# Optimization experiments

Measured on AMD Instinct MI355X. Metric: run time of the kernel, lower is better.

The kernel has to match this reference:

```python
import jax, jax.numpy as jnp
import numpy as np
from jax import lax

DN = ('NCHW', 'OIHW', 'NCHW')
EPS = 1e-9
MASK_THR = 1e-3


def box_filter(x, size):
    # Separable box (ones) filter with SAME padding; x: [1,1,H,W]
    pad = size // 2
    kv = jnp.ones((1, 1, size, 1), x.dtype)
    kh = jnp.ones((1, 1, 1, size), x.dtype)
    y = lax.conv_general_dilated(x, kv, (1, 1), [(pad, pad), (0, 0)], dimension_numbers=DN)
    return lax.conv_general_dilated(y, kh, (1, 1), [(0, 0), (pad, pad)], dimension_numbers=DN)


def setup_inputs() -> dict:
    key = jax.random.key(0)
    k1, k2, k3, k4 = jax.random.split(key, 4)
    H = W = 2048
    I = jax.random.uniform(k1, (1, 1, H, W), jnp.float32)            # image in [0,1]
    u = jax.random.uniform(k2, (1, 4, H, W), jnp.float32)            # class memberships
    b = 1.0 + 0.1 * jax.random.normal(k3, (1, 1, H, W), jnp.float32)  # bias field ~1
    e = jax.random.normal(k4, (1, 1, H, W), jnp.float32) * 0.1       # residual
    return {"I": I, "u": u, "b": b, "e": e, "p": 2, "size": 21}


def reference(I, u, b, e, p, size):
    C = u.shape[1]
    e_d = lax.stop_gradient(e)
    b_d = lax.stop_gradient(b)
    up = u ** p                      # [1,C,H,W]
    b2 = b_d * b_d
    mask = (I > MASK_THR).astype(I.dtype)
    norm = box_filter(mask, size)    # partialFilter: local valid-pixel count

    def filt(x):                     # convParFilt: mask-normalized local mean
        return box_filter(x, size) / (norm + EPS)

    b_K = filt(b)
    b2_K = filt(b2)

    # classCenter (vectorized over classes 1..C-1)
    A = (I - e_d) * b_K                                   # [1,1,H,W]
    num = jnp.sum(A * up[:, 1:], axis=(0, 2, 3))          # [C-1]
    den = jnp.sum(b2_K * up[:, 1:], axis=(0, 2, 3))       # [C-1]
    c0 = jnp.sum(I * up[:, :1]) / (jnp.sum(up[:, :1]) + EPS)
    v = jnp.concatenate([c0[None], num / (den + EPS)])    # [C]

    # bias-field update: convolution is linear, so sum over classes first
    vb = v[None, :, None, None]
    bd = filt((I - e_d) * jnp.sum(vb * up, axis=1, keepdims=True))
    db = filt(jnp.sum(vb * vb * up, axis=1, keepdims=True))
    bd = bd * mask + (1.0 - mask)
    db = db * mask + (1.0 - mask)
    b_new = bd / (db + EPS)
    diff = b - b_new
    return jnp.mean(diff * diff)
```

## Files before the change

### kernel.cpp

```cpp
#include <hip/hip_runtime.h>

constexpr int Hh = 2048;
constexpr int Ww = 2048;
constexpr int NN = Hh * Ww;
constexpr int W4 = Ww / 4;
constexpr int NN4 = NN / 4;
constexpr int RAD = 10;
constexpr float EPSf = 1e-9f;
constexpr float MASK_THRf = 0.001f;
constexpr int CH = 8;
constexpr int BH = 16;
constexpr int NB = Hh / BH;
constexpr int TOTW = NB * Ww;
constexpr int NSLOT = 32;

__device__ inline float rcpf(float x) { return __builtin_amdgcn_rcpf(x); }

__device__ inline float waveReduce(float v) {
    #pragma unroll
    for (int o = 32; o > 0; o >>= 1) v += __shfl_down(v, o, 64);
    return v;
}

__device__ inline float4 f4zero() { float4 z; z.x = z.y = z.z = z.w = 0.f; return z; }
__device__ inline float4 f4add(float4 a, float4 b) {
    float4 r; r.x = a.x + b.x; r.y = a.y + b.y; r.z = a.z + b.z; r.w = a.w + b.w; return r;
}
__device__ inline float4 f4sub(float4 a, float4 b) {
    float4 r; r.x = a.x - b.x; r.y = a.y - b.y; r.z = a.z - b.z; r.w = a.w - b.w; return r;
}
__device__ inline void add4(float4& a, const float4 b) { a.x += b.x; a.y += b.y; a.z += b.z; a.w += b.w; }

__device__ inline void scan4(float v0, float v1, float v2, float v3, int lane,
                             float& carry, float P[4]) {
    float s0 = v0, s1 = s0 + v1, s2 = s1 + v2, s3 = s2 + v3;
    float T = s3;
    #pragma unroll
    for (int o = 1; o < 64; o <<= 1) {
        float t = __shfl_up(T, o, 64);
        if (lane >= o) T += t;
    }
    float base = T - s3 + carry;
    P[0] = base + s0; P[1] = base + s1; P[2] = base + s2; P[3] = base + s3;
    carry += __shfl(T, 63, 64);
}

__device__ inline float4 boxExtract(const float Pp[4], const float Pc[4], const float Pn[4], int lane) {
    int l2 = (lane + 2) & 63, l3 = (lane + 3) & 63;
    int m3 = (lane - 3) & 63, m2 = (lane - 2) & 63;
    bool c2 = (lane + 2) < 64, c3 = (lane + 3) < 64;
    bool g3 = lane >= 3, g2 = lane >= 2;
    float hc0 = __shfl(Pc[2], l2, 64), hn0 = __shfl(Pn[2], l2, 64);
    float hc1 = __shfl(Pc[3], l2, 64), hn1 = __shfl(Pn[3], l2, 64);
    float hc2 = __shfl(Pc[0], l3, 64), hn2 = __shfl(Pn[0], l3, 64);
    float hc3 = __shfl(Pc[1], l3, 64), hn3 = __shfl(Pn[1], l3, 64);
    float lc0 = __shfl(Pc[1], m3, 64), lp0 = __shfl(Pp[1], m3, 64);
    float lc1 = __shfl(Pc[2], m3, 64), lp1 = __shfl(Pp[2], m3, 64);
    float lc2 = __shfl(Pc[3], m3, 64), lp2 = __shfl(Pp[3], m3, 64);
    float lc3 = __shfl(Pc[0], m2, 64), lp3 = __shfl(Pp[0], m2, 64);
    float4 r;
    r.x = (c2 ? hc0 : hn0) - (g3 ? lc0 : lp0);
    r.y = (c2 ? hc1 : hn1) - (g3 ? lc1 : lp1);
    r.z = (c3 ? hc2 : hn2) - (g3 ? lc2 : lp2);
    r.w = (c3 ? hc3 : hn3) - (g2 ? lc3 : lp3);
    return r;
}

__global__ __launch_bounds__(256) void k1p(
        const float* __restrict__ I, const float* __restrict__ B,
        float* __restrict__ vpm, float* __restrict__ vpb, float* __restrict__ vpb2,
        float* __restrict__ tm, float* __restrict__ tb, float* __restrict__ tb2) {
    int x4 = blockIdx.x * 256 + threadIdx.x;
    int y0 = blockIdx.y * BH;
    const float4* I4 = (const float4*)I;
    const float4* B4 = (const float4*)B;
    float4 am = f4zero(), ab = f4zero(), ab2 = f4zero();
    #pragma unroll
    for (int r = 0; r < BH; ++r) {
        int idx = (y0 + r) * W4 + x4;
        float4 iv = I4[idx], bv = B4[idx];
        am.x += (iv.x > MASK_THRf) ? 1.f : 0.f;
        am.y += (iv.y > MASK_THRf) ? 1.f : 0.f;
        am.z += (iv.z > MASK_THRf) ? 1.f : 0.f;
        am.w += (iv.w > MASK_THRf) ? 1.f : 0.f;
        ab.x += bv.x; ab.y += bv.y; ab.z += bv.z; ab.w += bv.w;
        ab2.x += bv.x * bv.x; ab2.y += bv.y * bv.y;
        ab2.z += bv.z * bv.z; ab2.w += bv.w * bv.w;
        ((float4*)vpm)[idx] = am;
        ((float4*)vpb)[idx] = ab;
        ((float4*)vpb2)[idx] = ab2;
    }
    int t = blockIdx.y * W4 + x4;
    ((float4*)tm)[t] = am; ((float4*)tb)[t] = ab; ((float4*)tb2)[t] = ab2;
}

__global__ __launch_bounds__(256) void koff(
        const float* __restrict__ t0, const float* __restrict__ t1, const float* __restrict__ t2,
        float* __restrict__ o0, float* __restrict__ o1, float* __restrict__ o2) {
    int col = blockIdx.x * 256 + threadIdx.x;
    const float4* t; float4* o;
    if (blockIdx.y == 0)      { t = (const float4*)t0; o = (float4*)o0; }
    else if (blockIdx.y == 1) { t = (const float4*)t1; o = (float4*)o1; }
    else                      { t = (const float4*)t2; o = (float4*)o2; }
    float4 acc = f4zero();
    #pragma unroll 8
    for (int b = 0; b < NB; ++b) {
        o[b * W4 + col] = acc;
        float4 v = t[b * W4 + col];
        add4(acc, v);
    }
}

#define VBOX3(cc, vA, vB, vC, PA, PB, PC, OA, OB, OC) do { \
    int xo_ = (cc) * 64 + lane; \
    float4 uA_ = PA[upBase + xo_], uB_ = PB[upBase + xo_], uC_ = PC[upBase + xo_]; \
    float4 oA_ = OA[obUp + xo_], oB_ = OB[obUp + xo_], oC_ = OC[obUp + xo_]; \
    float4 dA_ = f4zero(), dB_ = f4zero(), dC_ = f4zero(); \
    float4 eA_ = f4zero(), eB_ = f4zero(), eC_ = f4zero(); \
    if (hasDn) { dA_ = PA[dnBase + xo_]; dB_ = PB[dnBase + xo_]; dC_ = PC[dnBase + xo_]; \
                 eA_ = OA[obDn + xo_]; eB_ = OB[obDn + xo_]; eC_ = OC[obDn + xo_]; } \
    vA = f4sub(f4add(uA_, oA_), f4add(dA_, eA_)); \
    vB = f4sub(f4add(uB_, oB_), f4add(dB_, eB_)); \
    vC = f4sub(f4add(uC_, oC_), f4add(dC_, eC_)); } while (0)

__device__ inline void k2_pix(float bm, float bb, float bb2, float Iv, float ev,
                              float u0, float u1, float u2, float u3, float* a) {
    float rn = rcpf(bm + EPSf);
    float bK = bb * rn;
    float b2K = bb2 * rn;
    float p0 = u0 * u0, p1 = u1 * u1, p2 = u2 * u2, p3 = u3 * u3;
    a[0] += Iv * p0;
    a[1] += p0;
    float A = (Iv - ev) * bK;
    a[2] += A * p1; a[3] += A * p2; a[4] += A * p3;
    a[5] += b2K * p1; a[6] += b2K * p2; a[7] += b2K * p3;
}

__global__ __launch_bounds__(256) void k2h(
        const float* __restrict__ vpm, const float* __restrict__ vpb, const float* __restrict__ vpb2,
        const float* __restrict__ om, const float* __restrict__ ob, const float* __restrict__ ob2,
        const float* __restrict__ I, const float* __restrict__ E, const float* __restrict__ U,
        float* __restrict__ accA) {
    int row = (blockIdx.x * 256 + threadIdx.x) >> 6;
    int lane = threadIdx.x & 63;
    int yup = row + RAD; if (yup > Hh - 1) yup = Hh - 1;
    int ydn = row - RAD - 1;
    bool hasDn = ydn >= 0;
    int upBase = yup * W4;
    int dnBase = hasDn ? ydn * W4 : 0;
    int obUp = (yup / BH) * W4;
    int obDn = hasDn ? (ydn / BH) * W4 : 0;
    int rowBase = row * W4;

    const float4* Pm = (const float4*)vpm;
    const float4* Pb = (const float4*)vpb;
    const float4* Pq = (const float4*)vpb2;
    const float4* Om = (const float4*)om;
    const float4* Ob = (const float4*)ob;
    const float4* Oq = (const float4*)ob2;
    const float4* I4 = (const float4*)I;
    const float4* E4 = (const float4*)E;
    const float4* U0 = (const float4*)U;
    const float4* U1 = U0 + NN4;
    const float4* U2 = U1 + NN4;
    const float4* U3 = U2 + NN4;

    float cm = 0.f, cb = 0.f, cq = 0.f;
    float Pm_p[4] = {0, 0, 0, 0}, Pb_p[4] = {0, 0, 0, 0}, Pq_p[4] = {0, 0, 0, 0};
    float Pm_c[4], Pb_c[4], Pq_c[4], Pm_n[4], Pb_n[4], Pq_n[4];
    float a[8] = {0, 0, 0, 0, 0, 0, 0, 0};

    {
        float4 vm, vb, vq;
        VBOX3(0, vm, vb, vq, Pm, Pb, Pq, Om, Ob, Oq);
        scan4(vm.x, vm.y, vm.z, vm.w, lane, cm, Pm_c);
        scan4(vb.x, vb.y, vb.z, vb.w, lane, cb, Pb_c);
        scan4(vq.x, vq.y, vq.z, vq.w, lane, cq, Pq_c);
    }
    #pragma unroll 1
    for (int c = 0; c < CH; ++c) {
        int xo = rowBase + c * 64 + lane;
        float4 Iv = I4[xo], Ev = E4[xo];
        float4 u0 = U0[xo], u1 = U1[xo], u2 = U2[xo], u3 = U3[xo];
        if (c + 1 < CH) {
            float4 vm, vb, vq;
            VBOX3(c + 1, vm, vb, vq, Pm, Pb, Pq, Om, Ob, Oq);
            scan4(vm.x, vm.y, vm.z, vm.w, lane, cm, Pm_n);
            scan4(vb.x, vb.y, vb.z, vb.w, lane, cb, Pb_n);
            scan4(vq.x, vq.y, vq.z, vq.w, lane, cq, Pq_n);
        } else {
            #pragma unroll
            for (int e = 0; e < 4; ++e) { Pm_n[e] = cm; Pb_n[e] = cb; Pq_n[e] = cq; }
        }
        float4 bm = boxExtract(Pm_p, Pm_c, Pm_n, lane);
        float4 bb = boxExtract(Pb_p, Pb_c, Pb_n, lane);
        float4 bq = boxExtract(Pq_p, Pq_c, Pq_n, lane);
        k2_pix(bm.x, bb.x, bq.x, Iv.x, Ev.x, u0.x, u1.x, u2.x, u3.x, a);
        k2_pix(bm.y, bb.y, bq.y, Iv.y, Ev.y, u0.y, u1.y, u2.y, u3.y, a);
        k2_pix(bm.z, bb.z, bq.z, Iv.z, Ev.z, u0.z, u1.z, u2.z, u3.z, a);
        k2_pix(bm.w, bb.w, bq.w, Iv.w, Ev.w, u0.w, u1.w, u2.w, u3.w, a);
        #pragma unroll
        for (int e = 0; e < 4; ++e) {
            Pm_p[e] = Pm_c[e]; Pb_p[e] = Pb_c[e]; Pq_p[e] = Pq_c[e];
            Pm_c[e] = Pm_n[e]; Pb_c[e] = Pb_n[e]; Pq_c[e] = Pq_n[e];
        }
    }

    __shared__ float sred[4][8];
    int wave = threadIdx.x >> 6;
    #pragma unroll
    for (int k = 0; k < 8; ++k) a[k] = waveReduce(a[k]);
    if (lane == 0) {
        #pragma unroll
        for (int k = 0; k < 8; ++k) sred[wave][k] = a[k];
    }
    __syncthreads();
    if (threadIdx.x < 8) {
        float s = sred[0][threadIdx.x] + sred[1][threadIdx.x] +
                  sred[2][threadIdx.x] + sred[3][threadIdx.x];
        atomicAdd(&accA[threadIdx.x * NSLOT + (blockIdx.x & (NSLOT - 1))], s);
    }
}

__global__ void k3_v(const float* __restrict__ accA, float* __restrict__ vV) {
    int lane = threadIdx.x;
    float s[8];
    #pragma unroll
    for (int k = 0; k < 8; ++k) {
        float v = (lane < NSLOT) ? accA[k * NSLOT + lane] : 0.f;
        s[k] = waveReduce(v);
    }
    if (lane == 0) {
        vV[0] = s[0] / (s[1] + EPSf);
        vV[1] = s[2] / (s[5] + EPSf);
        vV[2] = s[3] / (s[6] + EPSf);
        vV[3] = s[4] / (s[7] + EPSf);
    }
}

__global__ __launch_bounds__(256) void k4p(
        const float* __restrict__ I, const float* __restrict__ E, const float* __restrict__ U,
        const float* __restrict__ vV,
        float* __restrict__ vpP, float* __restrict__ vpQ,
        float* __restrict__ tP, float* __restrict__ tQ) {
    int x4 = blockIdx.x * 256 + threadIdx.x;
    int y0 = blockIdx.y * BH;
    float v0 = vV[0], v1 = vV[1], v2 = vV[2], v3 = vV[3];
    float w0 = v0 * v0, w1 = v1 * v1, w2 = v2 * v2, w3 = v3 * v3;
    const float4* I4 = (const float4*)I;
    const float4* E4 = (const float4*)E;
    const float4* U0 = (const float4*)U;
    const float4* U1 = U0 + NN4;
    const float4* U2 = U1 + NN4;
    const float4* U3 = U2 + NN4;
    float4 aP = f4zero(), aQ = f4zero();
    #pragma unroll
    for (int r = 0; r < BH; ++r) {
        int idx = (y0 + r) * W4 + x4;
        float4 Iv = I4[idx], Ev = E4[idx];
        float4 a0 = U0[idx], a1 = U1[idx], a2 = U2[idx], a3 = U3[idx];
        float p0, p1, p2, p3;
        p0 = a0.x * a0.x; p1 = a1.x * a1.x; p2 = a2.x * a2.x; p3 = a3.x * a3.x;
        aP.x += (Iv.x - Ev.x) * (v0 * p0 + v1 * p1 + v2 * p2 + v3 * p3);
        aQ.x += w0 * p0 + w1 * p1 + w2 * p2 + w3 * p3;
        p0 = a0.y * a0.y; p1 = a1.y * a1.y; p2 = a2.y * a2.y; p3 = a3.y * a3.y;
        aP.y += (Iv.y - Ev.y) * (v0 * p0 + v1 * p1 + v2 * p2 + v3 * p3);
        aQ.y += w0 * p0 + w1 * p1 + w2 * p2 + w3 * p3;
        p0 = a0.z * a0.z; p1 = a1.z * a1.z; p2 = a2.z * a2.z; p3 = a3.z * a3.z;
        aP.z += (Iv.z - Ev.z) * (v0 * p0 + v1 * p1 + v2 * p2 + v3 * p3);
        aQ.z += w0 * p0 + w1 * p1 + w2 * p2 + w3 * p3;
        p0 = a0.w * a0.w; p1 = a1.w * a1.w; p2 = a2.w * a2.w; p3 = a3.w * a3.w;
        aP.w += (Iv.w - Ev.w) * (v0 * p0 + v1 * p1 + v2 * p2 + v3 * p3);
        aQ.w += w0 * p0 + w1 * p1 + w2 * p2 + w3 * p3;
        ((float4*)vpP)[idx] = aP;
        ((float4*)vpQ)[idx] = aQ;
    }
    int t = blockIdx.y * W4 + x4;
    ((float4*)tP)[t] = aP; ((float4*)tQ)[t] = aQ;
}

__global__ __launch_bounds__(256) void k5h(
        const float* __restrict__ vpP, const float* __restrict__ vpQ, const float* __restrict__ vpm,
        const float* __restrict__ oP, const float* __restrict__ oQ, const float* __restrict__ om,
        const float* __restrict__ I, const float* __restrict__ B,
        float* __restrict__ accL) {
    int row = (blockIdx.x * 256 + threadIdx.x) >> 6;
    int lane = threadIdx.x & 63;
    int yup = row + RAD; if (yup > Hh - 1) yup = Hh - 1;
    int ydn = row - RAD - 1;
    bool hasDn = ydn >= 0;
    int upBase = yup * W4;
    int dnBase = hasDn ? ydn * W4 : 0;
    int obUp = (yup / BH) * W4;
    int obDn = hasDn ? (ydn / BH) * W4 : 0;
    int rowBase = row * W4;

    const float4* Pp4 = (const float4*)vpP;
    const float4* Pq4 = (const float4*)vpQ;
    const float4* Pm4 = (const float4*)vpm;
    const float4* Op4 = (const float4*)oP;
    const float4* Oq4 = (const float4*)oQ;
    const float4* Om4 = (const float4*)om;
    const float4* I4 = (const float4*)I;
    const float4* B4 = (const float4*)B;

    float cP = 0.f, cQ = 0.f, cm = 0.f;
    float PP_p[4] = {0, 0, 0, 0}, PQ_p[4] = {0, 0, 0, 0}, PM_p[4] = {0, 0, 0, 0};
    float PP_c[4], PQ_c[4], PM_c[4], PP_n[4], PQ_n[4], PM_n[4];
    float a = 0.f;

    {
        float4 vP, vQ, vm;
        VBOX3(0, vP, vQ, vm, Pp4, Pq4, Pm4, Op4, Oq4, Om4);
        scan4(vP.x, vP.y, vP.z, vP.w, lane, cP, PP_c);
        scan4(vQ.x, vQ.y, vQ.z, vQ.w, lane, cQ, PQ_c);
        scan4(vm.x, vm.y, vm.z, vm.w, lane, cm, PM_c);
    }
    #pragma unroll 1
    for (int c = 0; c < CH; ++c) {
        int xo = rowBase + c * 64 + lane;
        float4 Iv = I4[xo], Bv = B4[xo];
        if (c + 1 < CH) {
            float4 vP, vQ, vm;
            VBOX3(c + 1, vP, vQ, vm, Pp4, Pq4, Pm4, Op4, Oq4, Om4);
            scan4(vP.x, vP.y, vP.z, vP.w, lane, cP, PP_n);
            scan4(vQ.x, vQ.y, vQ.z, vQ.w, lane, cQ, PQ_n);
            scan4(vm.x, vm.y, vm.z, vm.w, lane, cm, PM_n);
        } else {
            #pragma unroll
            for (int e = 0; e < 4; ++e) { PP_n[e] = cP; PQ_n[e] = cQ; PM_n[e] = cm; }
        }
        float4 bP = boxExtract(PP_p, PP_c, PP_n, lane);
        float4 bQ = boxExtract(PQ_p, PQ_c, PQ_n, lane);
        float4 bM = boxExtract(PM_p, PM_c, PM_n, lane);
        {
            float rn = rcpf(bM.x + EPSf);
            float bd = bP.x * rn, db = bQ.x * rn;
            float m = (Iv.x > MASK_THRf) ? 1.f : 0.f;
            bd = bd * m + (1.f - m); db = db * m + (1.f - m);
            float d = Bv.x - bd * rcpf(db + EPSf); a += d * d;
        }
        {
            float rn = rcpf(bM.y + EPSf);
            float bd = bP.y * rn, db = bQ.y * rn;
            float m = (Iv.y > MASK_THRf) ? 1.f : 0.f;
            bd = bd * m + (1.f - m); db = db * m + (1.f - m);
            float d = Bv.y - bd * rcpf(db + EPSf); a += d * d;
        }
        {
            float rn = rcpf(bM.z + EPSf);
            float bd = bP.z * rn, db = bQ.z * rn;
            float m = (Iv.z > MASK_THRf) ? 1.f : 0.f;
            bd = bd * m + (1.f - m); db = db * m + (1.f - m);
            float d = Bv.z - bd * rcpf(db + EPSf); a += d * d;
        }
        {
            float rn = rcpf(bM.w + EPSf);
            float bd = bP.w * rn, db = bQ.w * rn;
            float m = (Iv.w > MASK_THRf) ? 1.f : 0.f;
            bd = bd * m + (1.f - m); db = db * m + (1.f - m);
            float d = Bv.w - bd * rcpf(db + EPSf); a += d * d;
        }
        #pragma unroll
        for (int e = 0; e < 4; ++e) {
            PP_p[e] = PP_c[e]; PQ_p[e] = PQ_c[e]; PM_p[e] = PM_c[e];
            PP_c[e] = PP_n[e]; PQ_c[e] = PQ_n[e]; PM_c[e] = PM_n[e];
        }
    }

    a = waveReduce(a);
    __shared__ float sred[4];
    int wave = threadIdx.x >> 6;
    if (lane == 0) sred[wave] = a;
    __syncthreads();
    if (threadIdx.x == 0) {
        atomicAdd(&accL[blockIdx.x & (NSLOT - 1)], sred[0] + sred[1] + sred[2] + sred[3]);
    }
}

__global__ void k6_out(const float* __restrict__ accL, float* __restrict__ out) {
    int lane = threadIdx.x;
    float v = (lane < NSLOT) ? accL[lane] : 0.f;
    v = waveReduce(v);
    if (lane == 0) out[0] = v / (float)NN;
}

extern "C" void kernel_launch(void* const* d_in, const int* in_sizes, int n_in,
                              void* d_out, int out_size, void* d_ws, size_t ws_size,
                              hipStream_t stream) {
    const float* I = (const float*)d_in[0];
    const float* U = (const float*)d_in[1];
    const float* B = (const float*)d_in[2];
    const float* E = (const float*)d_in[3];

    float* vpm  = (float*)d_ws;
    float* vpb  = vpm + NN;
    float* vpb2 = vpb + NN;
    float* tm   = vpb2 + NN;
    float* tb   = tm + TOTW;
    float* tb2  = tb + TOTW;
    float* om   = tb2 + TOTW;
    float* ob   = om + TOTW;
    float* ob2  = ob + TOTW;
    float* accA = ob2 + TOTW;
    float* accL = accA + 8 * NSLOT;
    float* vV   = accL + NSLOT;

    hipMemsetAsync(accA, 0, (8 * NSLOT + NSLOT) * sizeof(float), stream);

    dim3 blk(256);
    dim3 gband(2, NB);
    int hblocks = Hh / 4;

    k1p<<<gband, blk, 0, stream>>>(I, B, vpm, vpb, vpb2, tm, tb, tb2);
    koff<<<dim3(2, 3), blk, 0, stream>>>(tm, tb, tb2, om, ob, ob2);
    k2h<<<hblocks, blk, 0, stream>>>(vpm, vpb, vpb2, om, ob, ob2, I, E, U, accA);
    k3_v<<<1, 64, 0, stream>>>(accA, vV);
    k4p<<<gband, blk, 0, stream>>>(I, E, U, vV, vpb, vpb2, tm, tb);
    koff<<<dim3(2, 2), blk, 0, stream>>>(tm, tb, tb2, ob, ob2, om);
    k5h<<<hblocks, blk, 0, stream>>>(vpb, vpb2, vpm, ob, ob2, om, I, B, accL);
    k6_out<<<1, 64, 0, stream>>>(accL, (float*)d_out);
}
```

Baseline: 238.9 us.

## Split each row's horizontal box pass across two waves and halve band height

The horizontal box/reduction kernels now give each row to two waves instead of one. Each wave handles half of the column chunks, and the second wave rebuilds the preceding chunk's prefix so its window stays correct. Band height drops from 16 to 8, and the offset prefix kernel now works in place, which removes the separate offset buffers. The goal is more wave-level parallelism and latency hiding in the main passes. The cost is some redundant neighbour-chunk loads and scans, plus a longer serial loop in the offset kernel.

```diff
diff --git a/kernel.cpp b/kernel.cpp
--- a/kernel.cpp
+++ b/kernel.cpp
@@ -9,7 +9,8 @@
 constexpr float EPSf = 1e-9f;
 constexpr float MASK_THRf = 0.001f;
 constexpr int CH = 8;
-constexpr int BH = 16;
+constexpr int SEGC = CH / 2;
+constexpr int BH = 8;
 constexpr int NB = Hh / BH;
 constexpr int TOTW = NB * Ww;
 constexpr int NSLOT = 32;
@@ -95,18 +96,17 @@
 }
 
 __global__ __launch_bounds__(256) void koff(
-        const float* __restrict__ t0, const float* __restrict__ t1, const float* __restrict__ t2,
-        float* __restrict__ o0, float* __restrict__ o1, float* __restrict__ o2) {
+        float* __restrict__ t0, float* __restrict__ t1, float* __restrict__ t2) {
     int col = blockIdx.x * 256 + threadIdx.x;
-    const float4* t; float4* o;
-    if (blockIdx.y == 0)      { t = (const float4*)t0; o = (float4*)o0; }
-    else if (blockIdx.y == 1) { t = (const float4*)t1; o = (float4*)o1; }
-    else                      { t = (const float4*)t2; o = (float4*)o2; }
+    float4* t;
+    if (blockIdx.y == 0)      t = (float4*)t0;
+    else if (blockIdx.y == 1) t = (float4*)t1;
+    else                      t = (float4*)t2;
     float4 acc = f4zero();
     #pragma unroll 8
     for (int b = 0; b < NB; ++b) {
-        o[b * W4 + col] = acc;
         float4 v = t[b * W4 + col];
+        t[b * W4 + col] = acc;
         add4(acc, v);
     }
 }
@@ -141,8 +141,11 @@
         const float* __restrict__ om, const float* __restrict__ ob, const float* __restrict__ ob2,
         const float* __restrict__ I, const float* __restrict__ E, const float* __restrict__ U,
         float* __restrict__ accA) {
-    int row = (blockIdx.x * 256 + threadIdx.x) >> 6;
+    int wid = (blockIdx.x * 256 + threadIdx.x) >> 6;
     int lane = threadIdx.x & 63;
+    int row = wid >> 1;
+    int seg = wid & 1;
+    int c0 = seg * SEGC;
     int yup = row + RAD; if (yup > Hh - 1) yup = Hh - 1;
     int ydn = row - RAD - 1;
     bool hasDn = ydn >= 0;
@@ -170,15 +173,23 @@
     float Pm_c[4], Pb_c[4], Pq_c[4], Pm_n[4], Pb_n[4], Pq_n[4];
     float a[8] = {0, 0, 0, 0, 0, 0, 0, 0};
 
+    if (seg > 0) {
+        float4 vm, vb, vq;
+        VBOX3(c0 - 1, vm, vb, vq, Pm, Pb, Pq, Om, Ob, Oq);
+        scan4(vm.x, vm.y, vm.z, vm.w, lane, cm, Pm_p);
+        scan4(vb.x, vb.y, vb.z, vb.w, lane, cb, Pb_p);
+        scan4(vq.x, vq.y, vq.z, vq.w, lane, cq, Pq_p);
+    }
     {
         float4 vm, vb, vq;
-        VBOX3(0, vm, vb, vq, Pm, Pb, Pq, Om, Ob, Oq);
+        VBOX3(c0, vm, vb, vq, Pm, Pb, Pq, Om, Ob, Oq);
         scan4(vm.x, vm.y, vm.z, vm.w, lane, cm, Pm_c);
         scan4(vb.x, vb.y, vb.z, vb.w, lane, cb, Pb_c);
         scan4(vq.x, vq.y, vq.z, vq.w, lane, cq, Pq_c);
     }
-    #pragma unroll 1
-    for (int c = 0; c < CH; ++c) {
+    #pragma unroll
+    for (int cc = 0; cc < SEGC; ++cc) {
+        int c = c0 + cc;
         int xo = rowBase + c * 64 + lane;
         float4 Iv = I4[xo], Ev = E4[xo];
         float4 u0 = U0[xo], u1 = U1[xo], u2 = U2[xo], u3 = U3[xo];
@@ -284,8 +295,11 @@
         const float* __restrict__ oP, const float* __restrict__ oQ, const float* __restrict__ om,
         const float* __restrict__ I, const float* __restrict__ B,
         float* __restrict__ accL) {
-    int row = (blockIdx.x * 256 + threadIdx.x) >> 6;
+    int wid = (blockIdx.x * 256 + threadIdx.x) >> 6;
     int lane = threadIdx.x & 63;
+    int row = wid >> 1;
+    int seg = wid & 1;
+    int c0 = seg * SEGC;
     int yup = row + RAD; if (yup > Hh - 1) yup = Hh - 1;
     int ydn = row - RAD - 1;
     bool hasDn = ydn >= 0;
@@ -309,15 +323,23 @@
     float PP_c[4], PQ_c[4], PM_c[4], PP_n[4], PQ_n[4], PM_n[4];
     float a = 0.f;
 
+    if (seg > 0) {
+        float4 vP, vQ, vm;
+        VBOX3(c0 - 1, vP, vQ, vm, Pp4, Pq4, Pm4, Op4, Oq4, Om4);
+        scan4(vP.x, vP.y, vP.z, vP.w, lane, cP, PP_p);
+        scan4(vQ.x, vQ.y, vQ.z, vQ.w, lane, cQ, PQ_p);
+        scan4(vm.x, vm.y, vm.z, vm.w, lane, cm, PM_p);
+    }
     {
         float4 vP, vQ, vm;
-        VBOX3(0, vP, vQ, vm, Pp4, Pq4, Pm4, Op4, Oq4, Om4);
+        VBOX3(c0, vP, vQ, vm, Pp4, Pq4, Pm4, Op4, Oq4, Om4);
         scan4(vP.x, vP.y, vP.z, vP.w, lane, cP, PP_c);
         scan4(vQ.x, vQ.y, vQ.z, vQ.w, lane, cQ, PQ_c);
         scan4(vm.x, vm.y, vm.z, vm.w, lane, cm, PM_c);
     }
-    #pragma unroll 1
-    for (int c = 0; c < CH; ++c) {
+    #pragma unroll
+    for (int cc = 0; cc < SEGC; ++cc) {
+        int c = c0 + cc;
         int xo = rowBase + c * 64 + lane;
         float4 Iv = I4[xo], Bv = B4[xo];
         if (c + 1 < CH) {
@@ -399,10 +421,7 @@
     float* tm   = vpb2 + NN;
     float* tb   = tm + TOTW;
     float* tb2  = tb + TOTW;
-    float* om   = tb2 + TOTW;
-    float* ob   = om + TOTW;
-    float* ob2  = ob + TOTW;
-    float* accA = ob2 + TOTW;
+    float* accA = tb2 + TOTW;
     float* accL = accA + 8 * NSLOT;
     float* vV   = accL + NSLOT;
 
@@ -410,14 +429,14 @@
 
     dim3 blk(256);
     dim3 gband(2, NB);
-    int hblocks = Hh / 4;
+    int hblocks = Hh * 2 / 4;
 
     k1p<<<gband, blk, 0, stream>>>(I, B, vpm, vpb, vpb2, tm, tb, tb2);
-    koff<<<dim3(2, 3), blk, 0, stream>>>(tm, tb, tb2, om, ob, ob2);
-    k2h<<<hblocks, blk, 0, stream>>>(vpm, vpb, vpb2, om, ob, ob2, I, E, U, accA);
+    koff<<<dim3(2, 3), blk, 0, stream>>>(tm, tb, tb2);
+    k2h<<<hblocks, blk, 0, stream>>>(vpm, vpb, vpb2, tm, tb, tb2, I, E, U, accA);
     k3_v<<<1, 64, 0, stream>>>(accA, vV);
-    k4p<<<gband, blk, 0, stream>>>(I, E, U, vV, vpb, vpb2, tm, tb);
-    koff<<<dim3(2, 2), blk, 0, stream>>>(tm, tb, tb2, ob, ob2, om);
-    k5h<<<hblocks, blk, 0, stream>>>(vpb, vpb2, vpm, ob, ob2, om, I, B, accL);
+    k4p<<<gband, blk, 0, stream>>>(I, E, U, vV, vpb, vpb2, tb, tb2);
+    koff<<<dim3(2, 2), blk, 0, stream>>>(tb, tb2, tb2);
+    k5h<<<hblocks, blk, 0, stream>>>(vpb, vpb2, vpm, tb, tb2, tm, I, B, accL);
     k6_out<<<1, 64, 0, stream>>>(accL, (float*)d_out);
 }
```

New measurement: 291.0 us. 21.8% more time.
